# Performance work log

Measured on AMD Instinct MI355X. Metric: run time of the kernel, lower is better.

The kernel has to match this reference:

```python
import jax, jax.numpy as jnp
import numpy as np

N_NODES = 100000
N_EDGES = 3200000
IN_C = 256
OUT_C = 64
NEG_SLOPE = 0.2  # leaky_relu alpha


def setup_inputs() -> dict:
    key = jax.random.key(0)
    k1, k2, k3, k4 = jax.random.split(key, 4)
    x = jax.random.normal(k1, (N_NODES, IN_C), dtype=jnp.float32)
    edge_index = jax.random.randint(k2, (2, N_EDGES), 0, N_NODES, dtype=jnp.int32)
    # xavier-ish scales
    W = jax.random.normal(k3, (OUT_C, IN_C), dtype=jnp.float32) * (1.0 / np.sqrt(IN_C))
    a = jax.random.normal(k4, (2 * OUT_C, 1), dtype=jnp.float32) * 0.1
    return {"x": x, "edge_index": edge_index, "W": W, "a": a, "num_nodes": N_NODES}


def reference(x, edge_index, W, a, num_nodes):
    # eval mode: dropout is identity
    # add self loops
    loop = jnp.arange(num_nodes, dtype=edge_index.dtype)
    row = jnp.concatenate([edge_index[0], loop])  # source nodes (x_j)
    col = jnp.concatenate([edge_index[1], loop])  # destination nodes (x_i)

    h = x @ W.T  # [N, out_c]

    # e = cat([x_i, x_j], 1) @ a  ==  (h @ a_i)[col] + (h @ a_j)[row]
    a_i = a[:OUT_C, 0]
    a_j = a[OUT_C:, 0]
    s_i = h @ a_i  # [N]
    s_j = h @ a_j  # [N]
    e = jax.nn.leaky_relu(s_i[col] + s_j[row], negative_slope=NEG_SLOPE)  # [E+N]

    # segment softmax over destination node (col)
    m = jax.ops.segment_max(e, col, num_segments=num_nodes)  # [N]
    ex = jnp.exp(e - m[col])
    denom = jax.ops.segment_sum(ex, col, num_segments=num_nodes)  # [N]
    alpha = ex / denom[col]  # [E+N]

    # scatter-add aggregation: out[col] += alpha * h[row]
    out = jax.ops.segment_sum(alpha[:, None] * h[row], col, num_segments=num_nodes)
    return out
```

## Files before the change

kernel.cpp:

```cpp
#include <hip/hip_runtime.h>
#include <hip/hip_bf16.h>
#include <cstddef>
#include <cstdint>

#define IN_C 256
#define OUT_C 64
#define NEG_SLOPE 0.2f
#define BKT2 512
#define PCHUNK 4096
#define MAXB 256
#define CAP 18432

typedef __attribute__((ext_vector_type(4))) float f32x4;
typedef __attribute__((ext_vector_type(2))) float f32x2;
typedef __attribute__((ext_vector_type(8))) short s16x8;

__device__ __forceinline__ float bf2f(ushort u)
{
    return __uint_as_float(((uint32_t)u) << 16);
}

__device__ __forceinline__ ushort f2bf(float f)
{
    uint32_t u = __float_as_uint(f);
    u += 0x7fffu + ((u >> 16) & 1u);
    return (ushort)(u >> 16);
}

__device__ __forceinline__ uint32_t pack_bf2(float f0, float f1)
{
    const uint32_t u0 = __float_as_uint(f0) + 0x8000u;
    const uint32_t u1 = __float_as_uint(f1) + 0x8000u;
    return (u1 & 0xffff0000u) | (u0 >> 16);
}

__device__ __forceinline__ float lrelu_exp(float t)
{
    return __expf(fmaxf(t, NEG_SLOPE * t));
}

__global__ __launch_bounds__(256) void wconv_kernel(
    const float* __restrict__ W, ushort* __restrict__ wfrag,
    int* __restrict__ cursor, int nb)
{
    if (blockIdx.x == 64) {
        const int i = threadIdx.x;
        if (i < nb) cursor[i] = i * CAP;
        return;
    }
    const int idx = blockIdx.x * 256 + threadIdx.x;
    const int j = idx & 7;
    const int l = (idx >> 3) & 63;
    const int n = (idx >> 9) & 3;
    const int t = idx >> 11;
    const int k   = t * 32 + ((l >> 4) << 3) + j;
    const int col = n * 16 + (l & 15);
    wfrag[idx] = f2bf(W[col * IN_C + k]);
}

__global__ __launch_bounds__(256) void fused_h_mfma(
    const float* __restrict__ x, const ushort* __restrict__ wfrag,
    const float* __restrict__ a, ushort* __restrict__ hb,
    float* __restrict__ s_i, float* __restrict__ s_j, int n_nodes)
{
    __shared__ ushort Bs[32 * 64 * 8];

    const int tid = threadIdx.x;
    for (int i = tid; i < 2048; i += 256)
        ((float4*)Bs)[i] = ((const float4*)wfrag)[i];
    __syncthreads();

    const int lane = tid & 63;
    const int wv   = tid >> 6;
    const int m    = lane & 15;
    const int quad = lane >> 4;

    const int base = blockIdx.x * 64 + wv * 16;
    int row = base + m;
    if (row >= n_nodes) row = n_nodes - 1;

    f32x4 acc0 = {0.f, 0.f, 0.f, 0.f};
    f32x4 acc1 = {0.f, 0.f, 0.f, 0.f};
    f32x4 acc2 = {0.f, 0.f, 0.f, 0.f};
    f32x4 acc3 = {0.f, 0.f, 0.f, 0.f};

    const float* xrow = x + (size_t)row * IN_C + quad * 8;

    #pragma unroll
    for (int t = 0; t < 8; ++t) {
        const float4 xa = *(const float4*)(xrow + t * 32);
        const float4 xb = *(const float4*)(xrow + t * 32 + 4);
        union { s16x8 v; uint32_t u[4]; } af;
        af.u[0] = pack_bf2(xa.x, xa.y);
        af.u[1] = pack_bf2(xa.z, xa.w);
        af.u[2] = pack_bf2(xb.x, xb.y);
        af.u[3] = pack_bf2(xb.z, xb.w);

        const s16x8 b0 = *(const s16x8*)(Bs + ((t * 4 + 0) * 64 + lane) * 8);
        const s16x8 b1 = *(const s16x8*)(Bs + ((t * 4 + 1) * 64 + lane) * 8);
        const s16x8 b2 = *(const s16x8*)(Bs + ((t * 4 + 2) * 64 + lane) * 8);
        const s16x8 b3 = *(const s16x8*)(Bs + ((t * 4 + 3) * 64 + lane) * 8);

        acc0 = __builtin_amdgcn_mfma_f32_16x16x32_bf16(af.v, b0, acc0, 0, 0, 0);
        acc1 = __builtin_amdgcn_mfma_f32_16x16x32_bf16(af.v, b1, acc1, 0, 0, 0);
        acc2 = __builtin_amdgcn_mfma_f32_16x16x32_bf16(af.v, b2, acc2, 0, 0, 0);
        acc3 = __builtin_amdgcn_mfma_f32_16x16x32_bf16(af.v, b3, acc3, 0, 0, 0);
    }

    const int c0 = lane & 15;
    const float ai0 = a[c0],      ai1 = a[c0 + 16], ai2 = a[c0 + 32], ai3 = a[c0 + 48];
    const float aj0 = a[64 + c0], aj1 = a[80 + c0], aj2 = a[96 + c0], aj3 = a[112 + c0];

    #pragma unroll
    for (int r = 0; r < 4; ++r) {
        const int rowr = base + quad * 4 + r;
        float pi = acc0[r] * ai0 + acc1[r] * ai1 + acc2[r] * ai2 + acc3[r] * ai3;
        float pj = acc0[r] * aj0 + acc1[r] * aj1 + acc2[r] * aj2 + acc3[r] * aj3;
        pi += __shfl_xor(pi, 1, 64);  pj += __shfl_xor(pj, 1, 64);
        pi += __shfl_xor(pi, 2, 64);  pj += __shfl_xor(pj, 2, 64);
        pi += __shfl_xor(pi, 4, 64);  pj += __shfl_xor(pj, 4, 64);
        pi += __shfl_xor(pi, 8, 64);  pj += __shfl_xor(pj, 8, 64);
        if (rowr < n_nodes) {
            ushort* hr = hb + (size_t)rowr * OUT_C + c0;
            hr[0]  = f2bf(acc0[r]);
            hr[16] = f2bf(acc1[r]);
            hr[32] = f2bf(acc2[r]);
            hr[48] = f2bf(acc3[r]);
            if (c0 == 0) { s_i[rowr] = pi; s_j[rowr] = pj; }
        }
    }
}

__global__ __launch_bounds__(256) void partition_kernel(
    const int* __restrict__ ei, int* __restrict__ cursor,
    uint32_t* __restrict__ rec, int n_edges, int nb)
{
    __shared__ int      hist[MAXB];
    __shared__ int      lbase[MAXB];
    __shared__ int      gbase[MAXB];
    __shared__ int      lcur[MAXB];
    __shared__ uint32_t srt[PCHUNK];
    __shared__ uint8_t  bmap[PCHUNK];

    const int tid  = threadIdx.x;
    const int base = blockIdx.x * PCHUNK;
    const int lim  = min(PCHUNK, n_edges - base);

    hist[tid] = 0;
    __syncthreads();

    int rA[PCHUNK / 256], cA[PCHUNK / 256];
    #pragma unroll
    for (int k = 0; k < PCHUNK / 256; ++k) {
        const int i = tid + (k << 8);
        if (i < lim) {
            rA[k] = __builtin_nontemporal_load(ei + base + i);
            cA[k] = __builtin_nontemporal_load(ei + n_edges + base + i);
            atomicAdd(&hist[(uint32_t)cA[k] >> 9], 1);
        }
    }
    __syncthreads();

    const int v = hist[tid];
    lbase[tid] = v;
    __syncthreads();
    for (int off = 1; off < 256; off <<= 1) {
        const int mine  = lbase[tid];
        const int other = (tid >= off) ? lbase[tid - off] : 0;
        __syncthreads();
        lbase[tid] = mine + other;
        __syncthreads();
    }
    const int excl = lbase[tid] - v;
    __syncthreads();
    lbase[tid] = excl;
    lcur[tid]  = excl;
    gbase[tid] = (tid < nb && v > 0) ? atomicAdd(&cursor[tid], v) : 0;
    __syncthreads();

    #pragma unroll
    for (int k = 0; k < PCHUNK / 256; ++k) {
        const int i = tid + (k << 8);
        if (i < lim) {
            const int r = rA[k];
            const int c = cA[k];
            const int b = (uint32_t)c >> 9;
            const int pos = atomicAdd(&lcur[b], 1);
            srt[pos]  = ((uint32_t)r << 9) | (uint32_t)(c & (BKT2 - 1));
            bmap[pos] = (uint8_t)b;
        }
    }
    __syncthreads();

    for (int i = tid; i < lim; i += 256) {
        const int b = bmap[i];
        rec[gbase[b] + (i - lbase[b])] = srt[i];
    }
}

__global__ __launch_bounds__(1024) void refine_kernel(
    uint32_t* __restrict__ rec, const int* __restrict__ cursor,
    int* __restrict__ nodeoff, int n_nodes, int nb)
{
    __shared__ uint32_t recs[CAP];
    __shared__ int hcnt[BKT2];
    __shared__ int lcur[BKT2];
    __shared__ int sscan[BKT2];

    const int b     = blockIdx.x;
    const int tid   = threadIdx.x;
    const int start = b * CAP;
    const int cnt   = min(cursor[b] - start, CAP);

    if (tid < BKT2) hcnt[tid] = 0;
    __syncthreads();

    const int cnt4 = cnt >> 2;
    for (int i = tid; i < cnt4; i += 1024) {
        const uint4 rv4 = ((const uint4*)(rec + start))[i];
        ((uint4*)recs)[i] = rv4;
        atomicAdd(&hcnt[rv4.x & (BKT2 - 1)], 1);
        atomicAdd(&hcnt[rv4.y & (BKT2 - 1)], 1);
        atomicAdd(&hcnt[rv4.z & (BKT2 - 1)], 1);
        atomicAdd(&hcnt[rv4.w & (BKT2 - 1)], 1);
    }
    for (int i = (cnt & ~3) + tid; i < cnt; i += 1024) {
        const uint32_t rv = rec[start + i];
        recs[i] = rv;
        atomicAdd(&hcnt[rv & (BKT2 - 1)], 1);
    }
    __syncthreads();

    if (tid < BKT2) sscan[tid] = hcnt[tid];
    __syncthreads();
    for (int off = 1; off < BKT2; off <<= 1) {
        int mine = 0, other = 0;
        if (tid < BKT2) {
            mine  = sscan[tid];
            other = (tid >= off) ? sscan[tid - off] : 0;
        }
        __syncthreads();
        if (tid < BKT2) sscan[tid] = mine + other;
        __syncthreads();
    }
    if (tid < BKT2) {
        const int myc  = hcnt[tid];
        const int excl = sscan[tid] - myc;
        lcur[tid] = excl;
        const int g = b * BKT2 + tid;
        if (g < n_nodes) nodeoff[g] = start + excl;
    }
    if (b == nb - 1 && tid == 0) nodeoff[n_nodes] = start + cnt;
    __syncthreads();

    for (int i = tid; i < cnt; i += 1024) {
        const uint32_t rv = recs[i];
        const int pos = atomicAdd(&lcur[rv & (BKT2 - 1)], 1);
        rec[start + pos] = rv;
    }
}

__global__ __launch_bounds__(256) void gather_kernel(
    const uint32_t* __restrict__ rec, const ushort* __restrict__ hb,
    const float* __restrict__ s_i, const float* __restrict__ s_j,
    const int* __restrict__ nodeoff, const int* __restrict__ cursor,
    float* __restrict__ out, int n_nodes)
{
    int wid = (int)((blockIdx.x * 256u + threadIdx.x) >> 6);
    wid = __builtin_amdgcn_readfirstlane(wid);
    if (wid >= n_nodes) return;
    const int lane = threadIdx.x & 63;
    const int g    = lane >> 3;
    const int l8   = lane & 7;
    const uint32_t loff = (uint32_t)(l8 << 4);

    const int o = nodeoff[wid];
    int oe;
    if ((wid & (BKT2 - 1)) == BKT2 - 1) {
        const int b = wid >> 9;
        oe = min(cursor[b], b * CAP + CAP);
    } else {
        oe = nodeoff[wid + 1];
    }

    const float si = s_i[wid];
    const char* hbB = (const char*)hb;

    f32x2 a01 = {0.f, 0.f}, a23 = {0.f, 0.f};
    f32x2 a45 = {0.f, 0.f}, a67 = {0.f, 0.f};
    float dsum = 0.f;

    int e = o;
    for (; e + 32 <= oe; e += 32) {
        uint32_t rv[4];
        #pragma unroll
        for (int q = 0; q < 4; ++q) rv[q] = rec[e + q * 8 + g];
        float sj[4]; uint32_t off[4];
        #pragma unroll
        for (int q = 0; q < 4; ++q) {
            sj[q]  = s_j[rv[q] >> 9];
            off[q] = ((rv[q] & 0xFFFFFE00u) >> 2) + loff;
        }
        uint4 hv[4];
        #pragma unroll
        for (int q = 0; q < 4; ++q) hv[q] = *(const uint4*)(hbB + off[q]);
        #pragma unroll
        for (int q = 0; q < 4; ++q) {
            const float t  = si + sj[q];
            const float ex = __expf(fmaxf(t, NEG_SLOPE * t));
            const f32x2 e2 = {ex, ex};
            f32x2 h;
            h[0] = __uint_as_float(hv[q].x << 16);
            h[1] = __uint_as_float(hv[q].x & 0xffff0000u);
            a01 += e2 * h;
            h[0] = __uint_as_float(hv[q].y << 16);
            h[1] = __uint_as_float(hv[q].y & 0xffff0000u);
            a23 += e2 * h;
            h[0] = __uint_as_float(hv[q].z << 16);
            h[1] = __uint_as_float(hv[q].z & 0xffff0000u);
            a45 += e2 * h;
            h[0] = __uint_as_float(hv[q].w << 16);
            h[1] = __uint_as_float(hv[q].w & 0xffff0000u);
            a67 += e2 * h;
            dsum += ex;
        }
    }
    for (; e + 8 <= oe; e += 8) {
        const uint32_t rv = rec[e + g];
        const float sjv = s_j[rv >> 9];
        const uint32_t off = ((rv & 0xFFFFFE00u) >> 2) + loff;
        const uint4 hv = *(const uint4*)(hbB + off);
        const float t  = si + sjv;
        const float ex = __expf(fmaxf(t, NEG_SLOPE * t));
        const f32x2 e2 = {ex, ex};
        f32x2 h;
        h[0] = __uint_as_float(hv.x << 16);
        h[1] = __uint_as_float(hv.x & 0xffff0000u);
        a01 += e2 * h;
        h[0] = __uint_as_float(hv.y << 16);
        h[1] = __uint_as_float(hv.y & 0xffff0000u);
        a23 += e2 * h;
        h[0] = __uint_as_float(hv.z << 16);
        h[1] = __uint_as_float(hv.z & 0xffff0000u);
        a45 += e2 * h;
        h[0] = __uint_as_float(hv.w << 16);
        h[1] = __uint_as_float(hv.w & 0xffff0000u);
        a67 += e2 * h;
        dsum += ex;
    }
    if (e < oe) {
        const int m = oe - e;
        const uint32_t rv = rec[e + (g < m ? g : m - 1)];
        const float sjv = s_j[rv >> 9];
        const uint32_t off = ((rv & 0xFFFFFE00u) >> 2) + loff;
        const uint4 hv = *(const uint4*)(hbB + off);
        const float t  = si + sjv;
        const float ex = (g < m) ? __expf(fmaxf(t, NEG_SLOPE * t)) : 0.f;
        const f32x2 e2 = {ex, ex};
        f32x2 h;
        h[0] = __uint_as_float(hv.x << 16);
        h[1] = __uint_as_float(hv.x & 0xffff0000u);
        a01 += e2 * h;
        h[0] = __uint_as_float(hv.y << 16);
        h[1] = __uint_as_float(hv.y & 0xffff0000u);
        a23 += e2 * h;
        h[0] = __uint_as_float(hv.z << 16);
        h[1] = __uint_as_float(hv.z & 0xffff0000u);
        a45 += e2 * h;
        h[0] = __uint_as_float(hv.w << 16);
        h[1] = __uint_as_float(hv.w & 0xffff0000u);
        a67 += e2 * h;
        dsum += ex;
    }

    #pragma unroll
    for (int s = 8; s <= 32; s <<= 1) {
        a01[0] += __shfl_xor(a01[0], s, 64);
        a01[1] += __shfl_xor(a01[1], s, 64);
        a23[0] += __shfl_xor(a23[0], s, 64);
        a23[1] += __shfl_xor(a23[1], s, 64);
        a45[0] += __shfl_xor(a45[0], s, 64);
        a45[1] += __shfl_xor(a45[1], s, 64);
        a67[0] += __shfl_xor(a67[0], s, 64);
        a67[1] += __shfl_xor(a67[1], s, 64);
        dsum   += __shfl_xor(dsum,   s, 64);
    }

    const float t0  = si + s_j[wid];
    const float ex0 = __expf(fmaxf(t0, NEG_SLOPE * t0));
    const uint4 hs = *(const uint4*)(hbB + (size_t)wid * 128 + loff);
    a01[0] += ex0 * __uint_as_float(hs.x << 16);
    a01[1] += ex0 * __uint_as_float(hs.x & 0xffff0000u);
    a23[0] += ex0 * __uint_as_float(hs.y << 16);
    a23[1] += ex0 * __uint_as_float(hs.y & 0xffff0000u);
    a45[0] += ex0 * __uint_as_float(hs.z << 16);
    a45[1] += ex0 * __uint_as_float(hs.z & 0xffff0000u);
    a67[0] += ex0 * __uint_as_float(hs.w << 16);
    a67[1] += ex0 * __uint_as_float(hs.w & 0xffff0000u);
    dsum += ex0;

    if (g == 0) {
        const float inv = 1.0f / dsum;
        f32x4 o4;
        o4[0] = a01[0] * inv;
        o4[1] = a01[1] * inv;
        o4[2] = a23[0] * inv;
        o4[3] = a23[1] * inv;
        float* op = out + (size_t)wid * OUT_C + (l8 << 3);
        __builtin_nontemporal_store(o4, (f32x4*)op);
        o4[0] = a45[0] * inv;
        o4[1] = a45[1] * inv;
        o4[2] = a67[0] * inv;
        o4[3] = a67[1] * inv;
        __builtin_nontemporal_store(o4, (f32x4*)(op + 4));
    }
}

extern "C" void kernel_launch(void* const* d_in, const int* in_sizes, int n_in,
                              void* d_out, int out_size, void* d_ws, size_t ws_size,
                              hipStream_t stream)
{
    const float* x  = (const float*)d_in[0];
    const int*   ei = (const int*)d_in[1];
    const float* W  = (const float*)d_in[2];
    const float* a  = (const float*)d_in[3];

    const int N  = in_sizes[0] / IN_C;
    const int E  = in_sizes[1] / 2;
    const int NB = (N + BKT2 - 1) / BKT2;

    float* out = (float*)d_out;

    char* ws = (char*)d_ws;
    ushort* hb      = (ushort*)ws;                ws += (size_t)N * OUT_C * 2;
    float*  s_i     = (float*)ws;                 ws += (size_t)N * 4;
    float*  s_j     = (float*)ws;                 ws += (size_t)N * 4;
    int*    cursor  = (int*)ws;                   ws += (size_t)MAXB * 4;
    int*    nodeoff = (int*)ws;                   ws += (size_t)(N + 1) * 4;
    ws = (char*)(((uintptr_t)ws + 15) & ~(uintptr_t)15);
    ushort* wfrag   = (ushort*)ws;                ws += 32 * 64 * 8 * 2;
    ws = (char*)(((uintptr_t)ws + 15) & ~(uintptr_t)15);
    uint32_t* rec   = (uint32_t*)ws;

    hipLaunchKernelGGL(wconv_kernel, dim3(65), dim3(256), 0, stream,
                       W, wfrag, cursor, NB);
    hipLaunchKernelGGL(fused_h_mfma, dim3((N + 63) / 64), dim3(256), 0, stream,
                       x, wfrag, a, hb, s_i, s_j, N);

    const int pblocks = (E + PCHUNK - 1) / PCHUNK;
    hipLaunchKernelGGL(partition_kernel, dim3(pblocks), dim3(256), 0, stream,
                       ei, cursor, rec, E, NB);

    hipLaunchKernelGGL(refine_kernel, dim3(NB), dim3(1024), 0, stream,
                       rec, cursor, nodeoff, N, NB);

    hipLaunchKernelGGL(gather_kernel, dim3((N + 3) / 4), dim3(256), 0, stream,
                       rec, hb, s_i, s_j, nodeoff, cursor, out, N);
}
```

Before: 294.1 us.

## Fuse per-bucket refine sort with gather, sorting edges in LDS

Replaces the separate refine and gather kernels with one kernel per 256-node bucket. Each bucket's edge records are counting-sorted into shared memory, and the block's 16 waves then aggregate attention-weighted features for 16 nodes each, reading edges straight from LDS. This drops the write-back of sorted records, the nodeoff array and one kernel launch. Buckets are halved and the partition kernel goes to 512 threads and 512 buckets to fit the LDS budget. The catch is far fewer, longer-lived waves (about 391 blocks), which risks poorer latency hiding and load imbalance across CUs during the random feature gathers.

```diff
diff --git a/kernel.cpp b/kernel.cpp
--- a/kernel.cpp
+++ b/kernel.cpp
@@ -6,20 +6,15 @@
 #define IN_C 256
 #define OUT_C 64
 #define NEG_SLOPE 0.2f
-#define BKT2 512
+#define BKT2 256
 #define PCHUNK 4096
-#define MAXB 256
-#define CAP 18432
+#define MAXB 512
+#define CAP 9728
 
 typedef __attribute__((ext_vector_type(4))) float f32x4;
 typedef __attribute__((ext_vector_type(2))) float f32x2;
 typedef __attribute__((ext_vector_type(8))) short s16x8;
 
-__device__ __forceinline__ float bf2f(ushort u)
-{
-    return __uint_as_float(((uint32_t)u) << 16);
-}
-
 __device__ __forceinline__ ushort f2bf(float f)
 {
     uint32_t u = __float_as_uint(f);
@@ -34,18 +29,12 @@
     return (u1 & 0xffff0000u) | (u0 >> 16);
 }
 
-__device__ __forceinline__ float lrelu_exp(float t)
-{
-    return __expf(fmaxf(t, NEG_SLOPE * t));
-}
-
 __global__ __launch_bounds__(256) void wconv_kernel(
     const float* __restrict__ W, ushort* __restrict__ wfrag,
     int* __restrict__ cursor, int nb)
 {
     if (blockIdx.x == 64) {
-        const int i = threadIdx.x;
-        if (i < nb) cursor[i] = i * CAP;
+        for (int i = threadIdx.x; i < nb; i += 256) cursor[i] = i * CAP;
         return;
     }
     const int idx = blockIdx.x * 256 + threadIdx.x;
@@ -131,7 +120,7 @@
     }
 }
 
-__global__ __launch_bounds__(256) void partition_kernel(
+__global__ __launch_bounds__(512) void partition_kernel(
     const int* __restrict__ ei, int* __restrict__ cursor,
     uint32_t* __restrict__ rec, int n_edges, int nb)
 {
@@ -140,7 +129,7 @@
     __shared__ int      gbase[MAXB];
     __shared__ int      lcur[MAXB];
     __shared__ uint32_t srt[PCHUNK];
-    __shared__ uint8_t  bmap[PCHUNK];
+    __shared__ uint16_t bmap[PCHUNK];
 
     const int tid  = threadIdx.x;
     const int base = blockIdx.x * PCHUNK;
@@ -149,14 +138,14 @@
     hist[tid] = 0;
     __syncthreads();
 
-    int rA[PCHUNK / 256], cA[PCHUNK / 256];
+    int rA[PCHUNK / 512], cA[PCHUNK / 512];
     #pragma unroll
-    for (int k = 0; k < PCHUNK / 256; ++k) {
-        const int i = tid + (k << 8);
+    for (int k = 0; k < PCHUNK / 512; ++k) {
+        const int i = tid + (k << 9);
         if (i < lim) {
             rA[k] = __builtin_nontemporal_load(ei + base + i);
             cA[k] = __builtin_nontemporal_load(ei + n_edges + base + i);
-            atomicAdd(&hist[(uint32_t)cA[k] >> 9], 1);
+            atomicAdd(&hist[(uint32_t)cA[k] >> 8], 1);
         }
     }
     __syncthreads();
@@ -164,7 +153,7 @@
     const int v = hist[tid];
     lbase[tid] = v;
     __syncthreads();
-    for (int off = 1; off < 256; off <<= 1) {
+    for (int off = 1; off < 512; off <<= 1) {
         const int mine  = lbase[tid];
         const int other = (tid >= off) ? lbase[tid - off] : 0;
         __syncthreads();
@@ -179,31 +168,33 @@
     __syncthreads();
 
     #pragma unroll
-    for (int k = 0; k < PCHUNK / 256; ++k) {
-        const int i = tid + (k << 8);
+    for (int k = 0; k < PCHUNK / 512; ++k) {
+        const int i = tid + (k << 9);
         if (i < lim) {
             const int r = rA[k];
             const int c = cA[k];
-            const int b = (uint32_t)c >> 9;
+            const int b = (uint32_t)c >> 8;
             const int pos = atomicAdd(&lcur[b], 1);
-            srt[pos]  = ((uint32_t)r << 9) | (uint32_t)(c & (BKT2 - 1));
-            bmap[pos] = (uint8_t)b;
-        }
-    }
-    __syncthreads();
-
-    for (int i = tid; i < lim; i += 256) {
+            srt[pos]  = ((uint32_t)r << 8) | (uint32_t)(c & (BKT2 - 1));
+            bmap[pos] = (uint16_t)b;
+        }
+    }
+    __syncthreads();
+
+    for (int i = tid; i < lim; i += 512) {
         const int b = bmap[i];
         rec[gbase[b] + (i - lbase[b])] = srt[i];
     }
 }
 
-__global__ __launch_bounds__(1024) void refine_kernel(
-    uint32_t* __restrict__ rec, const int* __restrict__ cursor,
-    int* __restrict__ nodeoff, int n_nodes, int nb)
-{
-    __shared__ uint32_t recs[CAP];
+__global__ __launch_bounds__(1024) void sortgather_kernel(
+    const uint32_t* __restrict__ rec, const ushort* __restrict__ hb,
+    const float* __restrict__ s_i, const float* __restrict__ s_j,
+    const int* __restrict__ cursor, float* __restrict__ out, int n_nodes)
+{
+    __shared__ uint32_t srt[CAP];
     __shared__ int hcnt[BKT2];
+    __shared__ int nstart[BKT2 + 1];
     __shared__ int lcur[BKT2];
     __shared__ int sscan[BKT2];
 
@@ -218,17 +209,13 @@
     const int cnt4 = cnt >> 2;
     for (int i = tid; i < cnt4; i += 1024) {
         const uint4 rv4 = ((const uint4*)(rec + start))[i];
-        ((uint4*)recs)[i] = rv4;
         atomicAdd(&hcnt[rv4.x & (BKT2 - 1)], 1);
         atomicAdd(&hcnt[rv4.y & (BKT2 - 1)], 1);
         atomicAdd(&hcnt[rv4.z & (BKT2 - 1)], 1);
         atomicAdd(&hcnt[rv4.w & (BKT2 - 1)], 1);
     }
-    for (int i = (cnt & ~3) + tid; i < cnt; i += 1024) {
-        const uint32_t rv = rec[start + i];
-        recs[i] = rv;
-        atomicAdd(&hcnt[rv & (BKT2 - 1)], 1);
-    }
+    for (int i = (cnt & ~3) + tid; i < cnt; i += 1024)
+        atomicAdd(&hcnt[rec[start + i] & (BKT2 - 1)], 1);
     __syncthreads();
 
     if (tid < BKT2) sscan[tid] = hcnt[tid];
@@ -244,175 +231,162 @@
         __syncthreads();
     }
     if (tid < BKT2) {
-        const int myc  = hcnt[tid];
-        const int excl = sscan[tid] - myc;
-        lcur[tid] = excl;
-        const int g = b * BKT2 + tid;
-        if (g < n_nodes) nodeoff[g] = start + excl;
-    }
-    if (b == nb - 1 && tid == 0) nodeoff[n_nodes] = start + cnt;
+        const int excl = sscan[tid] - hcnt[tid];
+        nstart[tid] = excl;
+        lcur[tid]   = excl;
+    }
+    if (tid == 0) nstart[BKT2] = cnt;
     __syncthreads();
 
     for (int i = tid; i < cnt; i += 1024) {
-        const uint32_t rv = recs[i];
-        const int pos = atomicAdd(&lcur[rv & (BKT2 - 1)], 1);
-        rec[start + pos] = rv;
-    }
-}
-
-__global__ __launch_bounds__(256) void gather_kernel(
-    const uint32_t* __restrict__ rec, const ushort* __restrict__ hb,
-    const float* __restrict__ s_i, const float* __restrict__ s_j,
-    const int* __restrict__ nodeoff, const int* __restrict__ cursor,
-    float* __restrict__ out, int n_nodes)
-{
-    int wid = (int)((blockIdx.x * 256u + threadIdx.x) >> 6);
-    wid = __builtin_amdgcn_readfirstlane(wid);
-    if (wid >= n_nodes) return;
-    const int lane = threadIdx.x & 63;
+        const uint32_t rv = rec[start + i];
+        srt[atomicAdd(&lcur[rv & (BKT2 - 1)], 1)] = rv;
+    }
+    __syncthreads();
+
+    const int lane = tid & 63;
+    const int wv   = tid >> 6;
     const int g    = lane >> 3;
     const int l8   = lane & 7;
     const uint32_t loff = (uint32_t)(l8 << 4);
-
-    const int o = nodeoff[wid];
-    int oe;
-    if ((wid & (BKT2 - 1)) == BKT2 - 1) {
-        const int b = wid >> 9;
-        oe = min(cursor[b], b * CAP + CAP);
-    } else {
-        oe = nodeoff[wid + 1];
-    }
-
-    const float si = s_i[wid];
     const char* hbB = (const char*)hb;
 
-    f32x2 a01 = {0.f, 0.f}, a23 = {0.f, 0.f};
-    f32x2 a45 = {0.f, 0.f}, a67 = {0.f, 0.f};
-    float dsum = 0.f;
-
-    int e = o;
-    for (; e + 32 <= oe; e += 32) {
-        uint32_t rv[4];
-        #pragma unroll
-        for (int q = 0; q < 4; ++q) rv[q] = rec[e + q * 8 + g];
-        float sj[4]; uint32_t off[4];
-        #pragma unroll
-        for (int q = 0; q < 4; ++q) {
-            sj[q]  = s_j[rv[q] >> 9];
-            off[q] = ((rv[q] & 0xFFFFFE00u) >> 2) + loff;
-        }
-        uint4 hv[4];
-        #pragma unroll
-        for (int q = 0; q < 4; ++q) hv[q] = *(const uint4*)(hbB + off[q]);
-        #pragma unroll
-        for (int q = 0; q < 4; ++q) {
-            const float t  = si + sj[q];
+    for (int k = 0; k < BKT2 / 16; ++k) {
+        const int nl   = wv * (BKT2 / 16) + k;
+        const int node = b * BKT2 + nl;
+        if (node >= n_nodes) break;
+        const int o  = nstart[nl];
+        const int oe = nstart[nl + 1];
+        const float si = s_i[node];
+
+        f32x2 a01 = {0.f, 0.f}, a23 = {0.f, 0.f};
+        f32x2 a45 = {0.f, 0.f}, a67 = {0.f, 0.f};
+        float dsum = 0.f;
+
+        int e = o;
+        for (; e + 32 <= oe; e += 32) {
+            uint32_t rv[4];
+            #pragma unroll
+            for (int q = 0; q < 4; ++q) rv[q] = srt[e + q * 8 + g];
+            float sj[4]; uint32_t off[4];
+            #pragma unroll
+            for (int q = 0; q < 4; ++q) {
+                sj[q]  = s_j[rv[q] >> 8];
+                off[q] = ((rv[q] & 0xFFFFFF00u) >> 1) + loff;
+            }
+            uint4 hv[4];
+            #pragma unroll
+            for (int q = 0; q < 4; ++q) hv[q] = *(const uint4*)(hbB + off[q]);
+            #pragma unroll
+            for (int q = 0; q < 4; ++q) {
+                const float t  = si + sj[q];
+                const float ex = __expf(fmaxf(t, NEG_SLOPE * t));
+                const f32x2 e2 = {ex, ex};
+                f32x2 h;
+                h[0] = __uint_as_float(hv[q].x << 16);
+                h[1] = __uint_as_float(hv[q].x & 0xffff0000u);
+                a01 += e2 * h;
+                h[0] = __uint_as_float(hv[q].y << 16);
+                h[1] = __uint_as_float(hv[q].y & 0xffff0000u);
+                a23 += e2 * h;
+                h[0] = __uint_as_float(hv[q].z << 16);
+                h[1] = __uint_as_float(hv[q].z & 0xffff0000u);
+                a45 += e2 * h;
+                h[0] = __uint_as_float(hv[q].w << 16);
+                h[1] = __uint_as_float(hv[q].w & 0xffff0000u);
+                a67 += e2 * h;
+                dsum += ex;
+            }
+        }
+        for (; e + 8 <= oe; e += 8) {
+            const uint32_t rv = srt[e + g];
+            const float sjv = s_j[rv >> 8];
+            const uint32_t off = ((rv & 0xFFFFFF00u) >> 1) + loff;
+            const uint4 hv = *(const uint4*)(hbB + off);
+            const float t  = si + sjv;
             const float ex = __expf(fmaxf(t, NEG_SLOPE * t));
             const f32x2 e2 = {ex, ex};
             f32x2 h;
-            h[0] = __uint_as_float(hv[q].x << 16);
-            h[1] = __uint_as_float(hv[q].x & 0xffff0000u);
+            h[0] = __uint_as_float(hv.x << 16);
+            h[1] = __uint_as_float(hv.x & 0xffff0000u);
             a01 += e2 * h;
-            h[0] = __uint_as_float(hv[q].y << 16);
-            h[1] = __uint_as_float(hv[q].y & 0xffff0000u);
+            h[0] = __uint_as_float(hv.y << 16);
+            h[1] = __uint_as_float(hv.y & 0xffff0000u);
             a23 += e2 * h;
-            h[0] = __uint_as_float(hv[q].z << 16);
-            h[1] = __uint_as_float(hv[q].z & 0xffff0000u);
+            h[0] = __uint_as_float(hv.z << 16);
+            h[1] = __uint_as_float(hv.z & 0xffff0000u);
             a45 += e2 * h;
-            h[0] = __uint_as_float(hv[q].w << 16);
-            h[1] = __uint_as_float(hv[q].w & 0xffff0000u);
+            h[0] = __uint_as_float(hv.w << 16);
+            h[1] = __uint_as_float(hv.w & 0xffff0000u);
             a67 += e2 * h;
             dsum += ex;
         }
-    }
-    for (; e + 8 <= oe; e += 8) {
-        const uint32_t rv = rec[e + g];
-        const float sjv = s_j[rv >> 9];
-        const uint32_t off = ((rv & 0xFFFFFE00u) >> 2) + loff;
-        const uint4 hv = *(const uint4*)(hbB + off);
-        const float t  = si + sjv;
-        const float ex = __expf(fmaxf(t, NEG_SLOPE * t));
-        const f32x2 e2 = {ex, ex};
-        f32x2 h;
-        h[0] = __uint_as_float(hv.x << 16);
-        h[1] = __uint_as_float(hv.x & 0xffff0000u);
-        a01 += e2 * h;
-        h[0] = __uint_as_float(hv.y << 16);
-        h[1] = __uint_as_float(hv.y & 0xffff0000u);
-        a23 += e2 * h;
-        h[0] = __uint_as_float(hv.z << 16);
-        h[1] = __uint_as_float(hv.z & 0xffff0000u);
-        a45 += e2 * h;
-        h[0] = __uint_as_float(hv.w << 16);
-        h[1] = __uint_as_float(hv.w & 0xffff0000u);
-        a67 += e2 * h;
-        dsum += ex;
-    }
-    if (e < oe) {
-        const int m = oe - e;
-        const uint32_t rv = rec[e + (g < m ? g : m - 1)];
-        const float sjv = s_j[rv >> 9];
-        const uint32_t off = ((rv & 0xFFFFFE00u) >> 2) + loff;
-        const uint4 hv = *(const uint4*)(hbB + off);
-        const float t  = si + sjv;
-        const float ex = (g < m) ? __expf(fmaxf(t, NEG_SLOPE * t)) : 0.f;
-        const f32x2 e2 = {ex, ex};
-        f32x2 h;
-        h[0] = __uint_as_float(hv.x << 16);
-        h[1] = __uint_as_float(hv.x & 0xffff0000u);
-        a01 += e2 * h;
-        h[0] = __uint_as_float(hv.y << 16);
-        h[1] = __uint_as_float(hv.y & 0xffff0000u);
-        a23 += e2 * h;
-        h[0] = __uint_as_float(hv.z << 16);
-        h[1] = __uint_as_float(hv.z & 0xffff0000u);
-        a45 += e2 * h;
-        h[0] = __uint_as_float(hv.w << 16);
-        h[1] = __uint_as_float(hv.w & 0xffff0000u);
-        a67 += e2 * h;
-        dsum += ex;
-    }
-
-    #pragma unroll
-    for (int s = 8; s <= 32; s <<= 1) {
-        a01[0] += __shfl_xor(a01[0], s, 64);
-        a01[1] += __shfl_xor(a01[1], s, 64);
-        a23[0] += __shfl_xor(a23[0], s, 64);
-        a23[1] += __shfl_xor(a23[1], s, 64);
-        a45[0] += __shfl_xor(a45[0], s, 64);
-        a45[1] += __shfl_xor(a45[1], s, 64);
-        a67[0] += __shfl_xor(a67[0], s, 64);
-        a67[1] += __shfl_xor(a67[1], s, 64);
-        dsum   += __shfl_xor(dsum,   s, 64);
-    }
-
-    const float t0  = si + s_j[wid];
-    const float ex0 = __expf(fmaxf(t0, NEG_SLOPE * t0));
-    const uint4 hs = *(const uint4*)(hbB + (size_t)wid * 128 + loff);
-    a01[0] += ex0 * __uint_as_float(hs.x << 16);
-    a01[1] += ex0 * __uint_as_float(hs.x & 0xffff0000u);
-    a23[0] += ex0 * __uint_as_float(hs.y << 16);
-    a23[1] += ex0 * __uint_as_float(hs.y & 0xffff0000u);
-    a45[0] += ex0 * __uint_as_float(hs.z << 16);
-    a45[1] += ex0 * __uint_as_float(hs.z & 0xffff0000u);
-    a67[0] += ex0 * __uint_as_float(hs.w << 16);
-    a67[1] += ex0 * __uint_as_float(hs.w & 0xffff0000u);
-    dsum += ex0;
-
-    if (g == 0) {
-        const float inv = 1.0f / dsum;
-        f32x4 o4;
-        o4[0] = a01[0] * inv;
-        o4[1] = a01[1] * inv;
-        o4[2] = a23[0] * inv;
-        o4[3] = a23[1] * inv;
-        float* op = out + (size_t)wid * OUT_C + (l8 << 3);
-        __builtin_nontemporal_store(o4, (f32x4*)op);
-        o4[0] = a45[0] * inv;
-        o4[1] = a45[1] * inv;
-        o4[2] = a67[0] * inv;
-        o4[3] = a67[1] * inv;
-        __builtin_nontemporal_store(o4, (f32x4*)(op + 4));
+        if (e < oe) {
+            const int m = oe - e;
+            const uint32_t rv = srt[e + (g < m ? g : m - 1)];
+            const float sjv = s_j[rv >> 8];
+            const uint32_t off = ((rv & 0xFFFFFF00u) >> 1) + loff;
+            const uint4 hv = *(const uint4*)(hbB + off);
+            const float t  = si + sjv;
+            const float ex = (g < m) ? __expf(fmaxf(t, NEG_SLOPE * t)) : 0.f;
+            const f32x2 e2 = {ex, ex};
+            f32x2 h;
+            h[0] = __uint_as_float(hv.x << 16);
+            h[1] = __uint_as_float(hv.x & 0xffff0000u);
+            a01 += e2 * h;
+            h[0] = __uint_as_float(hv.y << 16);
+            h[1] = __uint_as_float(hv.y & 0xffff0000u);
+            a23 += e2 * h;
+            h[0] = __uint_as_float(hv.z << 16);
+            h[1] = __uint_as_float(hv.z & 0xffff0000u);
+            a45 += e2 * h;
+            h[0] = __uint_as_float(hv.w << 16);
+            h[1] = __uint_as_float(hv.w & 0xffff0000u);
+            a67 += e2 * h;
+            dsum += ex;
+        }
+
+        #pragma unroll
+        for (int s = 8; s <= 32; s <<= 1) {
+            a01[0] += __shfl_xor(a01[0], s, 64);
+            a01[1] += __shfl_xor(a01[1], s, 64);
+            a23[0] += __shfl_xor(a23[0], s, 64);
+            a23[1] += __shfl_xor(a23[1], s, 64);
+            a45[0] += __shfl_xor(a45[0], s, 64);
+            a45[1] += __shfl_xor(a45[1], s, 64);
+            a67[0] += __shfl_xor(a67[0], s, 64);
+            a67[1] += __shfl_xor(a67[1], s, 64);
+            dsum   += __shfl_xor(dsum,   s, 64);
+        }
+
+        const float t0  = si + s_j[node];
+        const float ex0 = __expf(fmaxf(t0, NEG_SLOPE * t0));
+        const uint4 hs = *(const uint4*)(hbB + (size_t)node * 128 + loff);
+        a01[0] += ex0 * __uint_as_float(hs.x << 16);
+        a01[1] += ex0 * __uint_as_float(hs.x & 0xffff0000u);
+        a23[0] += ex0 * __uint_as_float(hs.y << 16);
+        a23[1] += ex0 * __uint_as_float(hs.y & 0xffff0000u);
+        a45[0] += ex0 * __uint_as_float(hs.z << 16);
+        a45[1] += ex0 * __uint_as_float(hs.z & 0xffff0000u);
+        a67[0] += ex0 * __uint_as_float(hs.w << 16);
+        a67[1] += ex0 * __uint_as_float(hs.w & 0xffff0000u);
+        dsum += ex0;
+
+        if (g == 0) {
+            const float inv = 1.0f / dsum;
+            f32x4 o4;
+            o4[0] = a01[0] * inv;
+            o4[1] = a01[1] * inv;
+            o4[2] = a23[0] * inv;
+            o4[3] = a23[1] * inv;
+            float* op = out + (size_t)node * OUT_C + (l8 << 3);
+            __builtin_nontemporal_store(o4, (f32x4*)op);
+            o4[0] = a45[0] * inv;
+            o4[1] = a45[1] * inv;
+            o4[2] = a67[0] * inv;
+            o4[3] = a67[1] * inv;
+            __builtin_nontemporal_store(o4, (f32x4*)(op + 4));
+        }
     }
 }
 
@@ -436,7 +410,6 @@
     float*  s_i     = (float*)ws;                 ws += (size_t)N * 4;
     float*  s_j     = (float*)ws;                 ws += (size_t)N * 4;
     int*    cursor  = (int*)ws;                   ws += (size_t)MAXB * 4;
-    int*    nodeoff = (int*)ws;                   ws += (size_t)(N + 1) * 4;
     ws = (char*)(((uintptr_t)ws + 15) & ~(uintptr_t)15);
     ushort* wfrag   = (ushort*)ws;                ws += 32 * 64 * 8 * 2;
     ws = (char*)(((uintptr_t)ws + 15) & ~(uintptr_t)15);
@@ -448,12 +421,9 @@
                        x, wfrag, a, hb, s_i, s_j, N);
 
     const int pblocks = (E + PCHUNK - 1) / PCHUNK;
-    hipLaunchKernelGGL(partition_kernel, dim3(pblocks), dim3(256), 0, stream,
+    hipLaunchKernelGGL(partition_kernel, dim3(pblocks), dim3(512), 0, stream,
                        ei, cursor, rec, E, NB);
 
-    hipLaunchKernelGGL(refine_kernel, dim3(NB), dim3(1024), 0, stream,
-                       rec, cursor, nodeoff, N, NB);
-
-    hipLaunchKernelGGL(gather_kernel, dim3((N + 3) / 4), dim3(256), 0, stream,
-                       rec, hb, s_i, s_j, nodeoff, cursor, out, N);
-}
+    hipLaunchKernelGGL(sortgather_kernel, dim3(NB), dim3(1024), 0, stream,
+                       rec, hb, s_i, s_j, cursor, out, N);
+}
```

Result: faster. 280.2 us (-4.7%).
